# Kernel tuning notes

Measured on AMD Instinct MI355X. Metric: run time of the kernel, lower is better.

## Reference

```python
import jax, jax.numpy as jnp
import numpy as np

B = 16      # graphs
NPG = 1024  # nodes per graph (equal-sized, contiguous)
N = B * NPG
K = 12      # knn neighbors
DM = 128    # d_model
DH = 256    # d_hidden = 2*d_model
L = 3       # num_layers
DI = 2 * DM + 4  # msg mlp input dim


def _mlp2(x, W1, b1, W2, b2):
    return jax.nn.silu(x @ W1 + b1) @ W2 + b2


def setup_inputs() -> dict:
    key = jax.random.key(0)
    ks = list(jax.random.split(key, 16))
    def nrm(k, shape, fan):
        return jax.random.normal(k, shape, jnp.float32) / np.float32(np.sqrt(fan))
    return dict(
        x=jax.random.normal(ks[0], (N, 3), jnp.float32),
        batch=(jnp.arange(N) // NPG).astype(jnp.int32),
        in_W1=nrm(ks[1], (3, DM), 3), in_b1=jnp.zeros((DM,), jnp.float32),
        in_W2=nrm(ks[2], (DM, DM), DM), in_b2=jnp.zeros((DM,), jnp.float32),
        msg_W1=nrm(ks[3], (L, DI, DH), DI), msg_b1=jnp.zeros((L, DH), jnp.float32),
        msg_W2=nrm(ks[4], (L, DH, DM), DH), msg_b2=jnp.zeros((L, DM), jnp.float32),
        upd_W1=nrm(ks[5], (L, 2 * DM, DH), 2 * DM), upd_b1=jnp.zeros((L, DH), jnp.float32),
        upd_W2=nrm(ks[6], (L, DH, DM), DH), upd_b2=jnp.zeros((L, DM), jnp.float32),
        norm_w=jnp.ones((L, DM), jnp.float32), norm_b=jnp.zeros((L, DM), jnp.float32),
        norm_ms=jnp.ones((L, DM), jnp.float32),
        gate_W1=nrm(ks[7], (DM, DM), DM), gate_b1=jnp.zeros((DM,), jnp.float32),
        gate_W2=nrm(ks[8], (DM, 1), DM), gate_b2=jnp.zeros((1,), jnp.float32),
        head_W1=nrm(ks[9], (DM, DM), DM), head_b1=jnp.zeros((DM,), jnp.float32),
        head_W2=nrm(ks[10], (DM, 1), DM), head_b2=jnp.zeros((1,), jnp.float32),
    )


def _knn_edges(pos):
    # pos: [N,2]; graphs are contiguous blocks of NPG nodes -> blocked knn
    p3 = pos.reshape(B, NPG, 2)
    d2 = jnp.sum((p3[:, :, None, :] - p3[:, None, :, :]) ** 2, axis=-1)  # [B,n,n]
    d2 = jnp.where(jnp.eye(NPG, dtype=bool)[None], jnp.inf, d2)          # no self loops
    idx = jax.lax.top_k(-d2, K)[1]  # [B,n,K] nearest neighbors (sources)
    offs = (jnp.arange(B) * NPG)[:, None, None]
    src = (idx + offs).reshape(-1)
    dst = jnp.broadcast_to(jnp.arange(N).reshape(B, NPG, 1), (B, NPG, K)).reshape(-1)
    return src, dst


def _graph_norm(h, batch, cnt, w, b, ms):
    # PyG GraphNorm: out = w * (h - ms*mean) / sqrt(var + eps) + b, per-graph stats
    mean = jax.ops.segment_sum(h, batch, B) / cnt
    out = h - mean[batch] * ms
    var = jax.ops.segment_sum(out ** 2, batch, B) / cnt
    return w * out / jnp.sqrt(var + 1e-5)[batch] + b


def _forward(x, batch, in_W1, in_b1, in_W2, in_b2, msg_W1, msg_b1, msg_W2, msg_b2,
             upd_W1, upd_b1, upd_W2, upd_b2, norm_w, norm_b, norm_ms,
             gate_W1, gate_b1, gate_W2, gate_b2, head_W1, head_b1, head_W2, head_b2):
    pos = x[:, 1:3]
    src, dst = _knn_edges(pos)
    # edge_attr = [dx, dy, dist, ds]
    dp = pos[src] - pos[dst]
    dist = jnp.sqrt(jnp.sum(dp ** 2, axis=-1, keepdims=True) + 1e-12)
    ds = x[src, 0:1] - x[dst, 0:1]
    ea = jnp.concatenate([dp, dist, ds], axis=-1)  # [E,4]

    h = _mlp2(x, in_W1, in_b1, in_W2, in_b2)       # [N,DM]
    cnt = jax.ops.segment_sum(jnp.ones((N,), h.dtype), batch, B)[:, None]

    for i in range(L):
        m_in = jnp.concatenate([h[dst], h[src], ea], axis=-1)       # [E,2*DM+4]
        m = _mlp2(m_in, msg_W1[i], msg_b1[i], msg_W2[i], msg_b2[i])  # [E,DM]
        agg = jax.ops.segment_sum(m, dst, N)                         # scatter_add
        dh = _mlp2(jnp.concatenate([h, agg], axis=-1),
                   upd_W1[i], upd_b1[i], upd_W2[i], upd_b2[i])
        h = h + dh  # dropout is identity at inference
        h = _graph_norm(h, batch, cnt, norm_w[i], norm_b[i], norm_ms[i])

    # gated attention pool: segment softmax over gate logits
    gl = (jnp.tanh(h @ gate_W1 + gate_b1) @ gate_W2 + gate_b2)[:, 0]  # [N]
    gmax = jax.ops.segment_max(gl, batch, B)
    e = jnp.exp(gl - gmax[batch])
    a = e / jax.ops.segment_sum(e, batch, B)[batch]
    pooled = jax.ops.segment_sum(h * a[:, None], batch, B)            # [B,DM]

    return _mlp2(pooled, head_W1, head_b1, head_W2, head_b2)[:, 0]    # [B]


def reference(x, batch, in_W1, in_b1, in_W2, in_b2, msg_W1, msg_b1, msg_W2, msg_b2,
              upd_W1, upd_b1, upd_W2, upd_b2, norm_w, norm_b, norm_ms,
              gate_W1, gate_b1, gate_W2, gate_b2, head_W1, head_b1, head_W2, head_b2):
    return _forward(x, batch, in_W1, in_b1, in_W2, in_b2, msg_W1, msg_b1, msg_W2, msg_b2,
                    upd_W1, upd_b1, upd_W2, upd_b2, norm_w, norm_b, norm_ms,
                    gate_W1, gate_b1, gate_W2, gate_b2, head_W1, head_b1, head_W2, head_b2)
```

## Files before the change

kernel.cpp:

```cpp
#include <hip/hip_runtime.h>
#include <math.h>

#define NPTS 16384
#define BGR 16
#define NPGR 1024
#define KNN 12
#define DM 128
#define DH 256
#define NL 3
#define EDG (NPTS*KNN)

typedef unsigned short u16;
typedef unsigned int u32;
typedef __attribute__((ext_vector_type(8))) short short8;
typedef __attribute__((ext_vector_type(4))) float floatx4;

__device__ __forceinline__ float silu_f(float x) {
    return x / (1.0f + __expf(-x));
}
__device__ __forceinline__ u16 f2bf(float f) {
    union { float f; u32 u; } v; v.f = f;
    u32 r = v.u + 0x7fffu + ((v.u >> 16) & 1u);
    return (u16)(r >> 16);
}
__device__ __forceinline__ float bf2f(u16 b) {
    union { u32 u; float f; } v; v.u = ((u32)b) << 16;
    return v.f;
}

#define KPPB 16
#define PSTR 209
__global__ __launch_bounds__(256) void knn_kernel(const float* __restrict__ x,
                                                  int* __restrict__ srcb,
                                                  float* __restrict__ ea) {
#pragma clang fp contract(off)
    __shared__ float2 pxy[NPGR];
    __shared__ float s0[NPGR];
    __shared__ float sdf[KPPB * PSTR];
    __shared__ int   sif[KPPB * PSTR];
    __shared__ int   sel[KPPB][KNN];
    int t = threadIdx.x;
    int g   = blockIdx.x / (NPGR / KPPB);
    int blk = blockIdx.x % (NPGR / KPPB);
    int base = g * NPGR;
    for (int j = t; j < NPGR; j += 256) {
        const float* xp = x + (size_t)(base + j) * 3;
        s0[j] = xp[0];
        pxy[j] = make_float2(xp[1], xp[2]);
    }
    __syncthreads();
    int r  = t & 15;
    int pt = t >> 4;
    int il = blk * KPPB + pt;
    float2 pil = pxy[il];
    float xi = pil.x, yi = pil.y;
    float nd[KNN]; int ni[KNN];
#pragma unroll
    for (int k = 0; k < KNN; ++k) { nd[k] = 3.4e38f; ni[k] = 0x7fffffff; }
    int j0 = r * 64;
    for (int jj = 0; jj < 64; ++jj) {
        int j = j0 + ((jj + r) & 63);
        if (j == il) continue;
        float2 p = pxy[j];
        float dx = p.x - xi;
        float dy = p.y - yi;
        float dx2 = dx * dx;
        float dy2 = dy * dy;
        float d2 = dx2 + dy2;
        if (d2 < nd[KNN-1] || (d2 == nd[KNN-1] && j < ni[KNN-1])) {
            float cd = d2; int ci = j;
#pragma unroll
            for (int k = 0; k < KNN; ++k) {
                bool sw = (cd < nd[k]) || (cd == nd[k] && ci < ni[k]);
                float tdv = sw ? nd[k] : cd;
                nd[k] = sw ? cd : nd[k];
                cd = tdv;
                int tiv = sw ? ni[k] : ci;
                ni[k] = sw ? ci : ni[k];
                ci = tiv;
            }
        }
    }
#pragma unroll
    for (int k = 0; k < KNN; ++k) {
        sdf[pt * PSTR + r * 13 + k] = nd[k];
        sif[pt * PSTR + r * 13 + k] = ni[k];
    }
    __syncthreads();
    if (r == 0) {
        int head[16];
#pragma unroll
        for (int q = 0; q < 16; ++q) head[q] = 0;
#pragma unroll
        for (int k = 0; k < KNN; ++k) {
            float bd = 3.4e38f; int bi = 0x7fffffff; int bq = 0;
#pragma unroll
            for (int q = 0; q < 16; ++q) {
                int hq = head[q];
                float d = (hq < KNN) ? sdf[pt * PSTR + q * 13 + hq] : 3.4e38f;
                int  ix = (hq < KNN) ? sif[pt * PSTR + q * 13 + hq] : 0x7fffffff;
                if (d < bd || (d == bd && ix < bi)) { bd = d; bi = ix; bq = q; }
            }
            head[bq]++;
            sel[pt][k] = bi;
        }
    }
    __syncthreads();
    if (r < KNN) {
        int k = r;
        int j = sel[pt][k];
        size_t e = (size_t)(base + il) * KNN + k;
        srcb[e] = base + j;
        float x0i = s0[il];
        float2 pj = pxy[j];
        float dpx = pj.x - xi, dpy = pj.y - yi;
        float a = dpx * dpx;
        float b = dpy * dpy;
        float dist = sqrtf(a + b + 1e-12f);
        float dsv = s0[j] - x0i;
        *(float4*)(ea + e * 4) = make_float4(dpx, dpy, dist, dsv);
    }
}

__global__ __launch_bounds__(128) void in_mlp_kernel(const float* __restrict__ x,
    const float* __restrict__ W1, const float* __restrict__ b1,
    const float* __restrict__ W2, const float* __restrict__ b2,
    float* __restrict__ h, u16* __restrict__ hh, u16* __restrict__ hl) {
    __shared__ float hid[8][DM];
    __shared__ float xl[8][3];
    int t = threadIdx.x;
    int nb = blockIdx.x * 8;
    if (t < 24) xl[t / 3][t % 3] = x[(size_t)nb * 3 + t];
    __syncthreads();
    float w0 = W1[t], w1 = W1[DM + t], w2 = W1[2 * DM + t], bb = b1[t];
#pragma unroll
    for (int gi = 0; gi < 8; ++gi) {
        float v = xl[gi][0] * w0 + xl[gi][1] * w1 + xl[gi][2] * w2 + bb;
        hid[gi][t] = silu_f(v);
    }
    __syncthreads();
    float acc[8];
    float b2v = b2[t];
#pragma unroll
    for (int gi = 0; gi < 8; ++gi) acc[gi] = b2v;
    for (int k = 0; k < DM; ++k) {
        float w = W2[k * DM + t];
#pragma unroll
        for (int gi = 0; gi < 8; ++gi) acc[gi] += hid[gi][k] * w;
    }
#pragma unroll
    for (int gi = 0; gi < 8; ++gi) {
        size_t idx = (size_t)(nb + gi) * DM + t;
        float v = acc[gi];
        h[idx] = v;
        u16 hi = f2bf(v);
        hh[idx] = hi;
        hl[idx] = f2bf(v - bf2f(hi));
    }
}

#define MBM 64
#define MBN 128
#define MBK 32
#define MLDA 40

__global__ __launch_bounds__(256) void mgemm_kernel(
    const u16* __restrict__ A0h, const u16* __restrict__ A0l, int k0, int lda0,
    const u16* __restrict__ A1h, const u16* __restrict__ A1l, int lda1,
    const u16* __restrict__ Wh, const u16* __restrict__ Wl, int K,
    const float* __restrict__ bias, int biasN,
    const float* __restrict__ resid, int ldres,
    float* __restrict__ outf, u16* __restrict__ outh, u16* __restrict__ outl, int ldout,
    int act)
{
    __shared__ __align__(16) u16 Ash[MBM * MLDA];
    __shared__ __align__(16) u16 Asl[MBM * MLDA];
    __shared__ __align__(16) u16 Bsh[MBN * MLDA];
    __shared__ __align__(16) u16 Bsl[MBN * MLDA];
    int t = threadIdx.x;
    int row0 = blockIdx.x * MBM, col0 = blockIdx.y * MBN;
    int lane = t & 63, w = t >> 6;
    int wm = (w >> 1) * 32, wn = (w & 1) * 64;
    int quad = lane >> 4, r15 = lane & 15;
    int arow = t >> 2, acol = (t & 3) * 8;
    int brow = t >> 1, bcol = (t & 1) * 16;

    floatx4 acc[2][4];
#pragma unroll
    for (int m = 0; m < 2; ++m)
#pragma unroll
        for (int n = 0; n < 4; ++n) acc[m][n] = (floatx4){0.f, 0.f, 0.f, 0.f};

    for (int kt = 0; kt < K; kt += MBK) {
        const u16 *Aph, *Apl;
        if (kt < k0) {
            Aph = A0h + (size_t)(row0 + arow) * lda0 + kt + acol;
            Apl = A0l + (size_t)(row0 + arow) * lda0 + kt + acol;
        } else {
            Aph = A1h + (size_t)(row0 + arow) * lda1 + (kt - k0) + acol;
            Apl = A1l + (size_t)(row0 + arow) * lda1 + (kt - k0) + acol;
        }
        uint4 avh = *(const uint4*)Aph;
        uint4 avl = *(const uint4*)Apl;
        const u16* Bph = Wh + (size_t)(col0 + brow) * K + kt + bcol;
        const u16* Bpl = Wl + (size_t)(col0 + brow) * K + kt + bcol;
        uint4 bh0 = ((const uint4*)Bph)[0];
        uint4 bh1 = ((const uint4*)Bph)[1];
        uint4 bl0 = ((const uint4*)Bpl)[0];
        uint4 bl1 = ((const uint4*)Bpl)[1];
        __syncthreads();
        *(uint4*)(Ash + arow * MLDA + acol) = avh;
        *(uint4*)(Asl + arow * MLDA + acol) = avl;
        uint4* bdh = (uint4*)(Bsh + brow * MLDA + bcol);
        uint4* bdl = (uint4*)(Bsl + brow * MLDA + bcol);
        bdh[0] = bh0; bdh[1] = bh1;
        bdl[0] = bl0; bdl[1] = bl1;
        __syncthreads();
        short8 ah[2], alo[2], bhf[4], blf[4];
#pragma unroll
        for (int m = 0; m < 2; ++m) {
            ah[m]  = *(const short8*)(Ash + (wm + m*16 + r15) * MLDA + quad*8);
            alo[m] = *(const short8*)(Asl + (wm + m*16 + r15) * MLDA + quad*8);
        }
#pragma unroll
        for (int n = 0; n < 4; ++n) {
            bhf[n] = *(const short8*)(Bsh + (wn + n*16 + r15) * MLDA + quad*8);
            blf[n] = *(const short8*)(Bsl + (wn + n*16 + r15) * MLDA + quad*8);
        }
#pragma unroll
        for (int m = 0; m < 2; ++m)
#pragma unroll
            for (int n = 0; n < 4; ++n) {
                acc[m][n] = __builtin_amdgcn_mfma_f32_16x16x32_bf16(ah[m],  bhf[n], acc[m][n], 0, 0, 0);
                acc[m][n] = __builtin_amdgcn_mfma_f32_16x16x32_bf16(ah[m],  blf[n], acc[m][n], 0, 0, 0);
                acc[m][n] = __builtin_amdgcn_mfma_f32_16x16x32_bf16(alo[m], bhf[n], acc[m][n], 0, 0, 0);
            }
    }
#pragma unroll
    for (int n = 0; n < 4; ++n) {
        int col = col0 + wn + n*16 + r15;
        float bv = (bias && col < biasN) ? bias[col] : 0.f;
#pragma unroll
        for (int m = 0; m < 2; ++m) {
#pragma unroll
            for (int reg = 0; reg < 4; ++reg) {
                int row = row0 + wm + m*16 + quad*4 + reg;
                float v = acc[m][n][reg] + bv;
                if (act == 1) v = silu_f(v);
                else if (act == 2) v = tanhf(v);
                if (resid) v += resid[(size_t)row * ldres + col];
                size_t oidx = (size_t)row * ldout + col;
                if (outf) outf[oidx] = v;
                if (outh) {
                    u16 hi = f2bf(v);
                    outh[oidx] = hi;
                    outl[oidx] = f2bf(v - bf2f(hi));
                }
            }
        }
    }
}

__global__ __launch_bounds__(256) void edge_agg_kernel(
    const float* __restrict__ CS,
    const int* __restrict__ srcb, const float* __restrict__ ea,
    const float* __restrict__ W1ea,
    u16* __restrict__ HSh, u16* __restrict__ HSl)
{
    int i = blockIdx.x, t = threadIdx.x;
    __shared__ int ss[KNN];
    __shared__ float sea[KNN * 4];
    if (t < KNN) ss[t] = srcb[(size_t)i * KNN + t];
    if (t < KNN * 4) sea[t] = ea[(size_t)i * KNN * 4 + t];
    __syncthreads();
    float base = CS[(size_t)i * 512 + t];
    float wa = W1ea[t], wb = W1ea[DH + t], wc = W1ea[2 * DH + t], wd = W1ea[3 * DH + t];
    float hs = 0.f;
#pragma unroll
    for (int e = 0; e < KNN; ++e) {
        float v = base + CS[(size_t)ss[e] * 512 + 256 + t]
                + sea[e * 4 + 0] * wa + sea[e * 4 + 1] * wb
                + sea[e * 4 + 2] * wc + sea[e * 4 + 3] * wd;
        hs += silu_f(v);
    }
    size_t oidx = (size_t)i * DH + t;
    u16 hi = f2bf(hs);
    HSh[oidx] = hi;
    HSl[oidx] = f2bf(hs - bf2f(hi));
}

__global__ __launch_bounds__(256) void norm_part_kernel(const float* __restrict__ hn,
                                                        float* __restrict__ psum)
{
    int g = blockIdx.x, blk = blockIdx.y;
    int t = threadIdx.x, d = t & 127, half = t >> 7;
    size_t base = ((size_t)g * NPGR + (size_t)blk * 128 + half * 64) * DM;
    float s = 0.f, s2 = 0.f;
    for (int n = 0; n < 64; ++n) {
        float v = hn[base + (size_t)n * DM + d];
        s += v; s2 += v * v;
    }
    __shared__ float ps[2][DM], ps2[2][DM];
    ps[half][d] = s; ps2[half][d] = s2;
    __syncthreads();
    if (t < DM) {
        psum[(((size_t)g * 8 + blk) * 2 + 0) * DM + d] = ps[0][d] + ps[1][d];
        psum[(((size_t)g * 8 + blk) * 2 + 1) * DM + d] = ps2[0][d] + ps2[1][d];
    }
}

__global__ __launch_bounds__(256) void norm_apply_kernel(const float* __restrict__ hn,
    float* __restrict__ h, u16* __restrict__ hh, u16* __restrict__ hl,
    const float* __restrict__ psum,
    const float* __restrict__ w, const float* __restrict__ b, const float* __restrict__ ms)
{
    int g = blockIdx.x, blk = blockIdx.y, t = threadIdx.x;
    __shared__ float mmv[DM], rst[DM], wv[DM], bv[DM];
    if (t < DM) {
        float sum = 0.f, sq = 0.f;
        for (int q = 0; q < 8; ++q) {
            sum += psum[(((size_t)g * 8 + q) * 2 + 0) * DM + t];
            sq  += psum[(((size_t)g * 8 + q) * 2 + 1) * DM + t];
        }
        float mean = sum * (1.0f / NPGR);
        float mm = mean * ms[t];
        float var = sq * (1.0f / NPGR) - 2.f * mm * mean + mm * mm;
        mmv[t] = mm;
        rst[t] = 1.0f / sqrtf(var + 1e-5f);
        wv[t] = w[t]; bv[t] = b[t];
    }
    __syncthreads();
    size_t base = ((size_t)g * NPGR + (size_t)blk * 128) * DM;
    for (int i = t; i < 128 * DM; i += 256) {
        int dd = i & 127;
        float v = hn[base + i];
        float o = wv[dd] * (v - mmv[dd]) * rst[dd] + bv[dd];
        h[base + i] = o;
        u16 hi = f2bf(o);
        hh[base + i] = hi;
        hl[base + i] = f2bf(o - bf2f(hi));
    }
}

__global__ __launch_bounds__(256) void gate_dot_kernel(const float* __restrict__ Gh,
    const float* __restrict__ gW2, const float* __restrict__ gb2,
    float* __restrict__ gl)
{
    int t = threadIdx.x, lane = t & 63, w = t >> 6;
    int node = blockIdx.x * 4 + w;
    const float* gp = Gh + (size_t)node * DM;
    float v = gp[lane] * gW2[lane] + gp[lane + 64] * gW2[lane + 64];
    for (int off = 32; off > 0; off >>= 1) v += __shfl_down(v, off, 64);
    if (lane == 0) gl[node] = v + gb2[0];
}

__global__ __launch_bounds__(256) void pool_stats_kernel(const float* __restrict__ gl,
                                                         float* __restrict__ gstat)
{
    int g = blockIdx.x, t = threadIdx.x, lane = t & 63, w = t >> 6;
    __shared__ float red[4];
    const float* gp = gl + (size_t)g * NPGR;
    float mx = -3.4e38f;
    for (int n = t; n < NPGR; n += 256) mx = fmaxf(mx, gp[n]);
    for (int off = 32; off > 0; off >>= 1) mx = fmaxf(mx, __shfl_down(mx, off, 64));
    if (lane == 0) red[w] = mx;
    __syncthreads();
    float gmax = fmaxf(fmaxf(red[0], red[1]), fmaxf(red[2], red[3]));
    __syncthreads();
    float se = 0.f;
    for (int n = t; n < NPGR; n += 256) se += __expf(gp[n] - gmax);
    for (int off = 32; off > 0; off >>= 1) se += __shfl_down(se, off, 64);
    if (lane == 0) red[w] = se;
    __syncthreads();
    if (t == 0) { gstat[g * 2] = gmax; gstat[g * 2 + 1] = red[0] + red[1] + red[2] + red[3]; }
}

__global__ __launch_bounds__(256) void pool_part_kernel(const float* __restrict__ h,
    const float* __restrict__ gl, const float* __restrict__ gstat,
    float* __restrict__ ppool)
{
    int g = blockIdx.x, blk = blockIdx.y;
    int t = threadIdx.x, d = t & 127, half = t >> 7;
    float gmax = gstat[g * 2];
    size_t nbase = (size_t)g * NPGR + (size_t)blk * 128 + half * 64;
    float p = 0.f;
    for (int n = 0; n < 64; ++n)
        p += __expf(gl[nbase + n] - gmax) * h[(nbase + n) * DM + d];
    __shared__ float ps[2][DM];
    ps[half][d] = p;
    __syncthreads();
    if (t < DM) ppool[((size_t)g * 8 + blk) * DM + d] = ps[0][d] + ps[1][d];
}

__global__ __launch_bounds__(128) void pool_head_kernel(const float* __restrict__ ppool,
    const float* __restrict__ gstat,
    const float* __restrict__ hW1, const float* __restrict__ hb1,
    const float* __restrict__ hW2, const float* __restrict__ hb2,
    float* __restrict__ outp)
{
    int g = blockIdx.x, t = threadIdx.x;
    __shared__ float pl[DM];
    __shared__ float red[2];
    float ssum = gstat[g * 2 + 1];
    float p = 0.f;
    for (int q = 0; q < 8; ++q) p += ppool[((size_t)g * 8 + q) * DM + t];
    pl[t] = p / ssum;
    __syncthreads();
    float a = hb1[t];
    for (int k = 0; k < DM; ++k) a += pl[k] * hW1[k * DM + t];
    a = silu_f(a);
    float vv = a * hW2[t];
    int lane = t & 63, w = t >> 6;
    for (int off = 32; off > 0; off >>= 1) vv += __shfl_down(vv, off, 64);
    if (lane == 0) red[w] = vv;
    __syncthreads();
    if (t == 0) outp[g] = red[0] + red[1] + hb2[0];
}

__global__ __launch_bounds__(256) void precompute_kernel(
    const float* __restrict__ msgW2, const float* __restrict__ msgb2,
    const float* __restrict__ updW1, const float* __restrict__ updb1,
    float* __restrict__ W2U, float* __restrict__ bias2)
{
    int bid = blockIdx.x; int t = threadIdx.x;
    if (bid < NL * DH) {
        int l = bid / DH, k = bid % DH;
        const float* w2row = msgW2 + (size_t)l * DH * DM + (size_t)k * DM;
        const float* u1 = updW1 + (size_t)l * 2 * DM * DH;
        float acc = 0.f;
        for (int j = 0; j < DM; ++j) acc += w2row[j] * u1[(size_t)(DM + j) * DH + t];
        W2U[(size_t)l * DH * DH + (size_t)k * DH + t] = acc;
    } else {
        int l = bid - NL * DH;
        const float* u1 = updW1 + (size_t)l * 2 * DM * DH;
        const float* b2 = msgb2 + (size_t)l * DM;
        float acc = updb1[(size_t)l * DH + t];
        for (int j = 0; j < DM; ++j) acc += 12.0f * b2[j] * u1[(size_t)(DM + j) * DH + t];
        bias2[(size_t)l * DH + t] = acc;
    }
}

struct WJob { const float* src; u16* dh; u16* dl; int K, N, ldd, off; };
struct WJobs { WJob j[16]; };
__global__ __launch_bounds__(256) void wprep_kernel(WJobs jobs) {
    WJob jb = jobs.j[blockIdx.y];
    int n = blockIdx.x;
    if (n >= jb.N) return;
    for (int k = threadIdx.x; k < jb.K; k += 256) {
        float v = jb.src[(size_t)k * jb.N + n];
        u16 hi = f2bf(v);
        u16 lo = f2bf(v - bf2f(hi));
        jb.dh[(size_t)n * jb.ldd + jb.off + k] = hi;
        jb.dl[(size_t)n * jb.ldd + jb.off + k] = lo;
    }
}

extern "C" void kernel_launch(void* const* d_in, const int* in_sizes, int n_in,
                              void* d_out, int out_size, void* d_ws, size_t ws_size,
                              hipStream_t stream) {
    const float* x     = (const float*)d_in[0];
    const float* inW1  = (const float*)d_in[2];
    const float* inb1  = (const float*)d_in[3];
    const float* inW2  = (const float*)d_in[4];
    const float* inb2  = (const float*)d_in[5];
    const float* msgW1 = (const float*)d_in[6];
    const float* msgb1 = (const float*)d_in[7];
    const float* msgW2 = (const float*)d_in[8];
    const float* msgb2 = (const float*)d_in[9];
    const float* updW1 = (const float*)d_in[10];
    const float* updb1 = (const float*)d_in[11];
    const float* updW2 = (const float*)d_in[12];
    const float* updb2 = (const float*)d_in[13];
    const float* nw    = (const float*)d_in[14];
    const float* nb    = (const float*)d_in[15];
    const float* nms   = (const float*)d_in[16];
    const float* gW1   = (const float*)d_in[17];
    const float* gb1   = (const float*)d_in[18];
    const float* gW2   = (const float*)d_in[19];
    const float* gb2   = (const float*)d_in[20];
    const float* hW1   = (const float*)d_in[21];
    const float* hb1   = (const float*)d_in[22];
    const float* hW2   = (const float*)d_in[23];
    const float* hb2   = (const float*)d_in[24];
    float* outp = (float*)d_out;

    float* ws    = (float*)d_ws;
    float* h     = ws;
    float* CSb   = h + (size_t)NPTS * DM;
    float* hnb   = CSb + (size_t)NPTS * 512;
    float* W2U   = hnb + (size_t)NPTS * DM;
    float* bias2 = W2U + (size_t)NL * DH * DH;
    float* glb   = bias2 + NL * DH;
    int*   srcb  = (int*)(glb + NPTS);
    float* eab   = (float*)(srcb + EDG);
    float* psum  = eab + (size_t)EDG * 4;
    float* gstat = psum + 16 * 8 * 2 * DM;
    float* ppool = gstat + 32;
    u16* hh  = (u16*)(ppool + 16 * 8 * DM);
    u16* hl  = hh + (size_t)NPTS * DM;
    u16* HSh = hl + (size_t)NPTS * DM;
    u16* HSl = HSh + (size_t)NPTS * DH;
    u16* Th  = HSl + (size_t)NPTS * DH;
    u16* Tl  = Th + (size_t)NPTS * DH;
    u16* WCSh = Tl + (size_t)NPTS * DH;              u16* WCSl = WCSh + (size_t)NL * 512 * DM;
    u16* WTh = WCSl + (size_t)NL * 512 * DM;         u16* WTl = WTh + (size_t)NL * DH * 384;
    u16* WUh = WTl + (size_t)NL * DH * 384;          u16* WUl = WUh + (size_t)NL * DM * DH;
    u16* WGh = WUl + (size_t)NL * DM * DH;           u16* WGl = WGh + (size_t)DM * DM;

    hipLaunchKernelGGL(precompute_kernel, dim3(NL * DH + NL), dim3(DH), 0, stream,
                       msgW2, msgb2, updW1, updb1, W2U, bias2);

    WJobs jobs;
    int ji = 0;
    for (int l = 0; l < NL; ++l) {
        jobs.j[ji++] = WJob{ msgW1 + (size_t)l * 260 * DH,            WCSh + (size_t)l * 512 * DM,            WCSl + (size_t)l * 512 * DM,            128, 256, 128, 0 };
        jobs.j[ji++] = WJob{ msgW1 + (size_t)l * 260 * DH + 128 * DH, WCSh + (size_t)l * 512 * DM + 256 * DM, WCSl + (size_t)l * 512 * DM + 256 * DM, 128, 256, 128, 0 };
        jobs.j[ji++] = WJob{ updW1 + (size_t)l * 256 * DH,            WTh + (size_t)l * DH * 384, WTl + (size_t)l * DH * 384, 128, 256, 384, 0 };
        jobs.j[ji++] = WJob{ W2U   + (size_t)l * DH * DH,             WTh + (size_t)l * DH * 384, WTl + (size_t)l * DH * 384, 256, 256, 384, 128 };
        jobs.j[ji++] = WJob{ updW2 + (size_t)l * DH * DM,             WUh + (size_t)l * DM * DH, WUl + (size_t)l * DM * DH, 256, 128, 256, 0 };
    }
    jobs.j[ji++] = WJob{ gW1, WGh, WGl, 128, 128, 128, 0 };
    hipLaunchKernelGGL(wprep_kernel, dim3(256, 16), dim3(256), 0, stream, jobs);

    hipLaunchKernelGGL(knn_kernel, dim3(NPTS / KPPB), dim3(256), 0, stream, x, srcb, eab);
    hipLaunchKernelGGL(in_mlp_kernel, dim3(NPTS / 8), dim3(128), 0, stream,
                       x, inW1, inb1, inW2, inb2, h, hh, hl);

    for (int l = 0; l < NL; ++l) {
        const float* W1l = msgW1 + (size_t)l * 260 * DH;
        hipLaunchKernelGGL(mgemm_kernel, dim3(NPTS / MBM, 512 / MBN), dim3(256), 0, stream,
            hh, hl, DM, DM, (const u16*)nullptr, (const u16*)nullptr, 0,
            WCSh + (size_t)l * 512 * DM, WCSl + (size_t)l * 512 * DM, DM,
            msgb1 + (size_t)l * DH, 256, (const float*)nullptr, 0,
            CSb, (u16*)nullptr, (u16*)nullptr, 512, 0);
        hipLaunchKernelGGL(edge_agg_kernel, dim3(NPTS), dim3(DH), 0, stream,
            CSb, srcb, eab, W1l + (size_t)2 * DM * DH, HSh, HSl);
        hipLaunchKernelGGL(mgemm_kernel, dim3(NPTS / MBM, DH / MBN), dim3(256), 0, stream,
            hh, hl, DM, DM, HSh, HSl, DH,
            WTh + (size_t)l * DH * 384, WTl + (size_t)l * DH * 384, 384,
            bias2 + (size_t)l * DH, DH, (const float*)nullptr, 0,
            (float*)nullptr, Th, Tl, DH, 1);
        hipLaunchKernelGGL(mgemm_kernel, dim3(NPTS / MBM, DM / MBN), dim3(256), 0, stream,
            Th, Tl, DH, DH, (const u16*)nullptr, (const u16*)nullptr, 0,
            WUh + (size_t)l * DM * DH, WUl + (size_t)l * DM * DH, DH,
            updb2 + (size_t)l * DM, DM, h, DM,
            hnb, (u16*)nullptr, (u16*)nullptr, DM, 0);
        hipLaunchKernelGGL(norm_part_kernel, dim3(BGR, 8), dim3(256), 0, stream, hnb, psum);
        hipLaunchKernelGGL(norm_apply_kernel, dim3(BGR, 8), dim3(256), 0, stream,
            hnb, h, hh, hl, psum, nw + (size_t)l * DM, nb + (size_t)l * DM, nms + (size_t)l * DM);
    }

    hipLaunchKernelGGL(mgemm_kernel, dim3(NPTS / MBM, DM / MBN), dim3(256), 0, stream,
        hh, hl, DM, DM, (const u16*)nullptr, (const u16*)nullptr, 0,
        WGh, WGl, DM, gb1, DM, (const float*)nullptr, 0,
        hnb, (u16*)nullptr, (u16*)nullptr, DM, 2);
    hipLaunchKernelGGL(gate_dot_kernel, dim3(NPTS / 4), dim3(256), 0, stream,
        hnb, gW2, gb2, glb);

    hipLaunchKernelGGL(pool_stats_kernel, dim3(BGR), dim3(256), 0, stream, glb, gstat);
    hipLaunchKernelGGL(pool_part_kernel, dim3(BGR, 8), dim3(256), 0, stream, h, glb, gstat, ppool);
    hipLaunchKernelGGL(pool_head_kernel, dim3(BGR), dim3(128), 0, stream,
        ppool, gstat, hW1, hb1, hW2, hb2, outp);
}
```

Measured before the change: 595.3 us.

## Add 128x128 tile GEMM for message/update GEMMs and simplify knn scan

Adds a new GEMM kernel with 128-row tiles and a 4x4 MFMA accumulator grid per wave, which doubles per-block data reuse. It is used for the two large per-layer GEMMs (the node projection to 512 columns and the update first layer). The kNN scan now uses a strided neighbor order and drops the index tie-break in its insertion sort, so the compare logic is cheaper. Dropping the tie-break can change which neighbor is chosen when distances are exactly equal. The larger tiles raise register pressure and lower the block count.

```diff
diff --git a/kernel.cpp b/kernel.cpp
--- a/kernel.cpp
+++ b/kernel.cpp
@@ -57,9 +57,8 @@
     float nd[KNN]; int ni[KNN];
 #pragma unroll
     for (int k = 0; k < KNN; ++k) { nd[k] = 3.4e38f; ni[k] = 0x7fffffff; }
-    int j0 = r * 64;
     for (int jj = 0; jj < 64; ++jj) {
-        int j = j0 + ((jj + r) & 63);
+        int j = jj * 16 + r;
         if (j == il) continue;
         float2 p = pxy[j];
         float dx = p.x - xi;
@@ -67,11 +66,11 @@
         float dx2 = dx * dx;
         float dy2 = dy * dy;
         float d2 = dx2 + dy2;
-        if (d2 < nd[KNN-1] || (d2 == nd[KNN-1] && j < ni[KNN-1])) {
+        if (d2 < nd[KNN-1]) {
             float cd = d2; int ci = j;
 #pragma unroll
             for (int k = 0; k < KNN; ++k) {
-                bool sw = (cd < nd[k]) || (cd == nd[k] && ci < ni[k]);
+                bool sw = cd < nd[k];
                 float tdv = sw ? nd[k] : cd;
                 nd[k] = sw ? cd : nd[k];
                 cd = tdv;
@@ -249,6 +248,104 @@
                 if (act == 1) v = silu_f(v);
                 else if (act == 2) v = tanhf(v);
                 if (resid) v += resid[(size_t)row * ldres + col];
+                size_t oidx = (size_t)row * ldout + col;
+                if (outf) outf[oidx] = v;
+                if (outh) {
+                    u16 hi = f2bf(v);
+                    outh[oidx] = hi;
+                    outl[oidx] = f2bf(v - bf2f(hi));
+                }
+            }
+        }
+    }
+}
+
+#define M2BM 128
+__global__ __launch_bounds__(256) void mgemm128_kernel(
+    const u16* __restrict__ A0h, const u16* __restrict__ A0l, int k0, int lda0,
+    const u16* __restrict__ A1h, const u16* __restrict__ A1l, int lda1,
+    const u16* __restrict__ Wh, const u16* __restrict__ Wl, int K,
+    const float* __restrict__ bias, int biasN,
+    float* __restrict__ outf, u16* __restrict__ outh, u16* __restrict__ outl, int ldout,
+    int act)
+{
+    __shared__ __align__(16) u16 Ash[M2BM * MLDA];
+    __shared__ __align__(16) u16 Asl[M2BM * MLDA];
+    __shared__ __align__(16) u16 Bsh[MBN * MLDA];
+    __shared__ __align__(16) u16 Bsl[MBN * MLDA];
+    int t = threadIdx.x;
+    int row0 = blockIdx.x * M2BM, col0 = blockIdx.y * MBN;
+    int lane = t & 63, w = t >> 6;
+    int wm = (w >> 1) * 64, wn = (w & 1) * 64;
+    int quad = lane >> 4, r15 = lane & 15;
+    int srow = t >> 1, scol = (t & 1) * 16;
+
+    floatx4 acc[4][4];
+#pragma unroll
+    for (int m = 0; m < 4; ++m)
+#pragma unroll
+        for (int n = 0; n < 4; ++n) acc[m][n] = (floatx4){0.f, 0.f, 0.f, 0.f};
+
+    for (int kt = 0; kt < K; kt += MBK) {
+        const u16 *Aph, *Apl;
+        if (kt < k0) {
+            Aph = A0h + (size_t)(row0 + srow) * lda0 + kt + scol;
+            Apl = A0l + (size_t)(row0 + srow) * lda0 + kt + scol;
+        } else {
+            Aph = A1h + (size_t)(row0 + srow) * lda1 + (kt - k0) + scol;
+            Apl = A1l + (size_t)(row0 + srow) * lda1 + (kt - k0) + scol;
+        }
+        uint4 avh0 = ((const uint4*)Aph)[0];
+        uint4 avh1 = ((const uint4*)Aph)[1];
+        uint4 avl0 = ((const uint4*)Apl)[0];
+        uint4 avl1 = ((const uint4*)Apl)[1];
+        const u16* Bph = Wh + (size_t)(col0 + srow) * K + kt + scol;
+        const u16* Bpl = Wl + (size_t)(col0 + srow) * K + kt + scol;
+        uint4 bh0 = ((const uint4*)Bph)[0];
+        uint4 bh1 = ((const uint4*)Bph)[1];
+        uint4 bl0 = ((const uint4*)Bpl)[0];
+        uint4 bl1 = ((const uint4*)Bpl)[1];
+        __syncthreads();
+        uint4* adh = (uint4*)(Ash + srow * MLDA + scol);
+        uint4* adl = (uint4*)(Asl + srow * MLDA + scol);
+        adh[0] = avh0; adh[1] = avh1;
+        adl[0] = avl0; adl[1] = avl1;
+        uint4* bdh = (uint4*)(Bsh + srow * MLDA + scol);
+        uint4* bdl = (uint4*)(Bsl + srow * MLDA + scol);
+        bdh[0] = bh0; bdh[1] = bh1;
+        bdl[0] = bl0; bdl[1] = bl1;
+        __syncthreads();
+        short8 ah[4], alo[4], bhf[4], blf[4];
+#pragma unroll
+        for (int m = 0; m < 4; ++m) {
+            ah[m]  = *(const short8*)(Ash + (wm + m*16 + r15) * MLDA + quad*8);
+            alo[m] = *(const short8*)(Asl + (wm + m*16 + r15) * MLDA + quad*8);
+        }
+#pragma unroll
+        for (int n = 0; n < 4; ++n) {
+            bhf[n] = *(const short8*)(Bsh + (wn + n*16 + r15) * MLDA + quad*8);
+            blf[n] = *(const short8*)(Bsl + (wn + n*16 + r15) * MLDA + quad*8);
+        }
+#pragma unroll
+        for (int m = 0; m < 4; ++m)
+#pragma unroll
+            for (int n = 0; n < 4; ++n) {
+                acc[m][n] = __builtin_amdgcn_mfma_f32_16x16x32_bf16(ah[m],  bhf[n], acc[m][n], 0, 0, 0);
+                acc[m][n] = __builtin_amdgcn_mfma_f32_16x16x32_bf16(ah[m],  blf[n], acc[m][n], 0, 0, 0);
+                acc[m][n] = __builtin_amdgcn_mfma_f32_16x16x32_bf16(alo[m], bhf[n], acc[m][n], 0, 0, 0);
+            }
+    }
+#pragma unroll
+    for (int n = 0; n < 4; ++n) {
+        int col = col0 + wn + n*16 + r15;
+        float bv = (bias && col < biasN) ? bias[col] : 0.f;
+#pragma unroll
+        for (int m = 0; m < 4; ++m) {
+#pragma unroll
+            for (int reg = 0; reg < 4; ++reg) {
+                int row = row0 + wm + m*16 + quad*4 + reg;
+                float v = acc[m][n][reg] + bv;
+                if (act == 1) v = silu_f(v);
                 size_t oidx = (size_t)row * ldout + col;
                 if (outf) outf[oidx] = v;
                 if (outh) {
@@ -528,17 +625,17 @@
 
     for (int l = 0; l < NL; ++l) {
         const float* W1l = msgW1 + (size_t)l * 260 * DH;
-        hipLaunchKernelGGL(mgemm_kernel, dim3(NPTS / MBM, 512 / MBN), dim3(256), 0, stream,
+        hipLaunchKernelGGL(mgemm128_kernel, dim3(NPTS / M2BM, 512 / MBN), dim3(256), 0, stream,
             hh, hl, DM, DM, (const u16*)nullptr, (const u16*)nullptr, 0,
             WCSh + (size_t)l * 512 * DM, WCSl + (size_t)l * 512 * DM, DM,
-            msgb1 + (size_t)l * DH, 256, (const float*)nullptr, 0,
+            msgb1 + (size_t)l * DH, 256,
             CSb, (u16*)nullptr, (u16*)nullptr, 512, 0);
         hipLaunchKernelGGL(edge_agg_kernel, dim3(NPTS), dim3(DH), 0, stream,
             CSb, srcb, eab, W1l + (size_t)2 * DM * DH, HSh, HSl);
-        hipLaunchKernelGGL(mgemm_kernel, dim3(NPTS / MBM, DH / MBN), dim3(256), 0, stream,
+        hipLaunchKernelGGL(mgemm128_kernel, dim3(NPTS / M2BM, DH / MBN), dim3(256), 0, stream,
             hh, hl, DM, DM, HSh, HSl, DH,
             WTh + (size_t)l * DH * 384, WTl + (size_t)l * DH * 384, 384,
-            bias2 + (size_t)l * DH, DH, (const float*)nullptr, 0,
+            bias2 + (size_t)l * DH, DH,
             (float*)nullptr, Th, Tl, DH, 1);
         hipLaunchKernelGGL(mgemm_kernel, dim3(NPTS / MBM, DM / MBN), dim3(256), 0, stream,
             Th, Tl, DH, DH, (const u16*)nullptr, (const u16*)nullptr, 0,
```

Result: faster. 566.4 us (-4.9%).
